# Kernel optimization log

Measured on AMD Instinct MI355X. Metric: run time of the kernel, lower is better.

Reference implementation:

```python
import jax, jax.numpy as jnp
import numpy as np

# static config (matches init_kwargs and spatial_shapes input)
SPATIAL = ((100, 100), (50, 50), (25, 25), (13, 13))  # (H, W) per level
D_MODEL, N_HEADS, N_LEVELS, N_POINTS, D_FFN = 256, 8, 4, 4, 1024
D_HEAD = D_MODEL // N_HEADS
LEN_IN = sum(h * w for h, w in SPATIAL)
LEVEL_START = np.cumsum([0] + [h * w for h, w in SPATIAL])[:-1]


def setup_inputs() -> dict:
    key = jax.random.key(0)
    ks = jax.random.split(key, 12)
    N = 2
    f = lambda k, shape, s=0.02: jax.random.normal(k, shape, jnp.float32) * s
    return {
        "src": jax.random.normal(ks[0], (N, LEN_IN, D_MODEL), jnp.float32),
        "pos": jax.random.normal(ks[1], (N, LEN_IN, D_MODEL), jnp.float32),
        "reference_points": jax.random.uniform(ks[2], (N, LEN_IN, N_LEVELS, 2), jnp.float32),
        "spatial_shapes": jnp.asarray(SPATIAL, jnp.int32),
        "level_start_index": jnp.asarray(LEVEL_START, jnp.int32),
        "W_value": f(ks[3], (D_MODEL, D_MODEL)),
        "b_value": jnp.zeros((D_MODEL,), jnp.float32),
        "W_off": f(ks[4], (D_MODEL, N_HEADS * N_LEVELS * N_POINTS * 2)),
        "b_off": f(ks[5], (N_HEADS * N_LEVELS * N_POINTS * 2,), 0.5),
        "W_attn": f(ks[6], (D_MODEL, N_HEADS * N_LEVELS * N_POINTS)),
        "b_attn": jnp.zeros((N_HEADS * N_LEVELS * N_POINTS,), jnp.float32),
        "W_out": f(ks[7], (D_MODEL, D_MODEL)),
        "b_out": jnp.zeros((D_MODEL,), jnp.float32),
        "W1": f(ks[8], (D_MODEL, D_FFN)),
        "b1": jnp.zeros((D_FFN,), jnp.float32),
        "W2": f(ks[9], (D_FFN, D_MODEL)),
        "b2": jnp.zeros((D_MODEL,), jnp.float32),
        "g1": jnp.ones((D_MODEL,), jnp.float32),
        "be1": jnp.zeros((D_MODEL,), jnp.float32),
        "g2": jnp.ones((D_MODEL,), jnp.float32),
        "be2": jnp.zeros((D_MODEL,), jnp.float32),
    }


def _ln(x, g, b, eps=1e-5):
    mu = x.mean(-1, keepdims=True)
    var = ((x - mu) ** 2).mean(-1, keepdims=True)
    return (x - mu) * jax.lax.rsqrt(var + eps) * g + b


def _bilinear(v, loc, H, W):
    # v: [N, heads, H*W, Dh]; loc: [N, Lq, heads, P, 2] normalized to [0,1]
    # replicates F.grid_sample(align_corners=False, padding_mode='zeros') with grid=2*loc-1
    N, Lq, Hh, P, _ = loc.shape
    x = loc[..., 0] * W - 0.5
    y = loc[..., 1] * H - 0.5
    x0 = jnp.floor(x)
    y0 = jnp.floor(y)
    wx1 = x - x0
    wy1 = y - y0
    x0i = x0.astype(jnp.int32)
    y0i = y0.astype(jnp.int32)
    out = jnp.zeros((N, Lq, Hh, P, v.shape[-1]), v.dtype)
    for dy, dx in ((0, 0), (0, 1), (1, 0), (1, 1)):
        xi = x0i + dx
        yi = y0i + dy
        w = (wx1 if dx else 1.0 - wx1) * (wy1 if dy else 1.0 - wy1)
        valid = (xi >= 0) & (xi < W) & (yi >= 0) & (yi < H)
        idx = jnp.clip(yi, 0, H - 1) * W + jnp.clip(xi, 0, W - 1)  # [N,Lq,Hh,P]
        idx = idx.transpose(0, 2, 1, 3).reshape(N, Hh, Lq * P)
        g = jax.vmap(jax.vmap(lambda vm, im: vm[im]))(v, idx)  # [N,Hh,Lq*P,Dh]
        g = g.reshape(N, Hh, Lq, P, -1).transpose(0, 2, 1, 3, 4)
        out = out + (w * valid)[..., None] * g
    return out


def reference(src, pos, reference_points, spatial_shapes, level_start_index,
              W_value, b_value, W_off, b_off, W_attn, b_attn, W_out, b_out,
              W1, b1, W2, b2, g1, be1, g2, be2):
    N, Lq, _ = src.shape
    value = (src @ W_value + b_value).reshape(N, Lq, N_HEADS, D_HEAD)
    q = src + pos  # with_pos_embed
    off = (q @ W_off + b_off).reshape(N, Lq, N_HEADS, N_LEVELS, N_POINTS, 2)
    attn = (q @ W_attn + b_attn).reshape(N, Lq, N_HEADS, N_LEVELS * N_POINTS)
    attn = jax.nn.softmax(attn, axis=-1).reshape(N, Lq, N_HEADS, N_LEVELS, N_POINTS)
    # offset_normalizer = (W, H) per level
    normalizer = jnp.asarray([[w, h] for h, w in SPATIAL], jnp.float32)
    loc = reference_points[:, :, None, :, None, :] + off / normalizer[None, None, None, :, None, :]
    out = jnp.zeros((N, Lq, N_HEADS, D_HEAD), jnp.float32)
    for l, (H, W) in enumerate(SPATIAL):
        s = int(LEVEL_START[l])
        v_l = value[:, s:s + H * W].transpose(0, 2, 1, 3)  # [N, heads, H*W, Dh]
        samp = _bilinear(v_l, loc[:, :, :, l], H, W)       # [N, Lq, heads, P, Dh]
        out = out + jnp.einsum('nqhp,nqhpc->nqhc', attn[:, :, :, l], samp)
    src2 = out.reshape(N, Lq, D_MODEL) @ W_out + b_out
    x = _ln(src + src2, g1, be1)
    ffn = jax.nn.relu(x @ W1 + b1) @ W2 + b2
    return _ln(x + ffn, g2, be2)
```

## Files before the change

kernel.cpp:

```cpp
#include <hip/hip_runtime.h>
#include <hip/hip_bf16.h>
#include <cstdint>

#define D_MODEL   256
#define N_HEADS   8
#define N_LEVELS  4
#define N_POINTS  4
#define D_FFN     1024
#define D_HEAD    32
#define LEN_IN    13294
#define NBATCH    2
#define M_TOK     (NBATCH * LEN_IN)
#define M_PAD     26624

__constant__ int c_lvl_h[4] = {100, 50, 25, 13};
__constant__ int c_lvl_w[4] = {100, 50, 25, 13};
__constant__ int c_lvl_s[4] = {0, 10000, 12500, 13125};

typedef __attribute__((ext_vector_type(8))) __bf16 bf16x8;
typedef __attribute__((ext_vector_type(4))) __bf16 bf16x4;
typedef __attribute__((ext_vector_type(4))) float  f32x4;
typedef __attribute__((ext_vector_type(4))) uint32_t u32x4;

__device__ __forceinline__ float bflo(uint32_t w) { return __uint_as_float(w << 16); }
__device__ __forceinline__ float bfhi(uint32_t w) { return __uint_as_float(w & 0xffff0000u); }

__device__ __forceinline__ void lds_direct16(const void* g, void* l) {
    __builtin_amdgcn_global_load_lds(
        (const __attribute__((address_space(1))) uint32_t*)(uintptr_t)g,
        (__attribute__((address_space(3))) uint32_t*)(uintptr_t)l,
        16, 0, 0);
}

__global__ __launch_bounds__(256) void prep(
    const float* __restrict__ s0, const float* __restrict__ s1, const float* __restrict__ s2,
    const float* __restrict__ s3, const float* __restrict__ s4, const float* __restrict__ s5,
    __bf16* __restrict__ d0, __bf16* __restrict__ d1, __bf16* __restrict__ d2,
    __bf16* __restrict__ d3, __bf16* __restrict__ d4, __bf16* __restrict__ d5,
    const float* __restrict__ b_off, const float* __restrict__ b_attn,
    float* __restrict__ bias_oa,
    const float4* __restrict__ src, const float4* __restrict__ pos,
    bf16x4* __restrict__ sb, bf16x4* __restrict__ qb, int n4)
{
    const int tid = threadIdx.x;
    const int b = blockIdx.x;
    if (b >= 737) {
        const int i = (b - 737) * 256 + tid;
        if (i >= n4) return;
        const float4 s = src[i];
        const float4 p = pos[i];
        bf16x4 sv = { (__bf16)s.x, (__bf16)s.y, (__bf16)s.z, (__bf16)s.w };
        bf16x4 qv = { (__bf16)(s.x + p.x), (__bf16)(s.y + p.y),
                      (__bf16)(s.z + p.z), (__bf16)(s.w + p.w) };
        sb[i] = sv;
        qb[i] = qv;
        return;
    }
    if (b == 736) {
        if (tid < 256) bias_oa[tid] = b_off[tid];
        if (tid < 128) bias_oa[256 + tid] = b_attn[tid];
        return;
    }
    const int tx = tid & 31;
    const int ty = tid >> 5;
    const int starts[7] = {0, 64, 128, 160, 224, 480, 736};
    const int Ks[6] = {256, 256, 256, 256, 256, 1024};
    const int Ns[6] = {256, 256, 128, 256, 1024, 256};
    const float* srcs[6] = {s0, s1, s2, s3, s4, s5};
    __bf16* dsts[6] = {d0, d1, d2, d3, d4, d5};
    int i = 0;
    while (b >= starts[i + 1]) ++i;
    const int t = b - starts[i];
    const int K = Ks[i], N = Ns[i];
    const float* W = srcs[i];
    __bf16* Wt = dsts[i];
    const int ntx = N >> 5;
    const int n0 = (t % ntx) * 32;
    const int k0 = (t / ntx) * 32;

    __shared__ float tl[32][33];
    #pragma unroll
    for (int j = 0; j < 4; ++j)
        tl[ty + j * 8][tx] = W[(size_t)(k0 + ty + j * 8) * N + n0 + tx];
    __syncthreads();
    #pragma unroll
    for (int j = 0; j < 4; ++j)
        Wt[(size_t)(n0 + ty + j * 8) * K + k0 + tx] = (__bf16)tl[tx][ty + j * 8];
}

template <bool RELU, int K>
__device__ __forceinline__ void gemm_core(
    const __bf16* __restrict__ A, const __bf16* __restrict__ Bt,
    const float* __restrict__ bias, __bf16* __restrict__ C,
    int M, int N, int bm, int bn)
{
    __shared__ __bf16 smem[17408];
    __bf16* As = smem;
    __bf16* Bs = smem + 8192;

    const int tid  = threadIdx.x;
    const int lane = tid & 63;
    const int wv   = tid >> 6;
    const int wm   = (wv >> 1) * 64;
    const int wn   = (wv & 1) * 64;
    const int srow = lane >> 2;
    const int skc  = (lane & 3) * 8;
    const int fm   = lane & 15;
    const int fko  = (lane >> 4) * 8;

    f32x4 acc[4][4] = {};

    for (int k0 = 0; k0 < K; k0 += 64) {
        #pragma unroll
        for (int p = 0; p < 2; ++p) {
            #pragma unroll
            for (int c = 0; c < 2; ++c) {
                const int r = wv * 32 + c * 16;
                lds_direct16(A  + (size_t)(bm + r + srow) * K + k0 + p * 32 + skc, As + p * 4096 + r * 32);
                lds_direct16(Bt + (size_t)(bn + r + srow) * K + k0 + p * 32 + skc, Bs + p * 4096 + r * 32);
            }
        }
        __syncthreads();

        #pragma unroll
        for (int p = 0; p < 2; ++p) {
            bf16x8 af[4], bfr[4];
            #pragma unroll
            for (int t = 0; t < 4; ++t) {
                af[t]  = *(const bf16x8*)(As + p * 4096 + (wm + t * 16 + fm) * 32 + fko);
                bfr[t] = *(const bf16x8*)(Bs + p * 4096 + (wn + t * 16 + fm) * 32 + fko);
            }
            #pragma unroll
            for (int mt = 0; mt < 4; ++mt)
                #pragma unroll
                for (int nt = 0; nt < 4; ++nt)
                    acc[mt][nt] = __builtin_amdgcn_mfma_f32_16x16x32_bf16(
                        af[mt], bfr[nt], acc[mt][nt], 0, 0, 0);
        }
        __syncthreads();
    }

    const int ecol = lane & 15;
    const int erow = (lane >> 4) * 4;
    #pragma unroll
    for (int nt = 0; nt < 4; ++nt) {
        const int cl = wn + nt * 16 + ecol;
        const float bv = bias[bn + cl];
        #pragma unroll
        for (int mt = 0; mt < 4; ++mt) {
            #pragma unroll
            for (int r = 0; r < 4; ++r) {
                const int rl = wm + mt * 16 + erow + r;
                float v = acc[mt][nt][r] + bv;
                if (RELU) v = fmaxf(v, 0.f);
                smem[rl * 136 + cl] = (__bf16)v;
            }
        }
    }
    __syncthreads();
    #pragma unroll
    for (int rr = 0; rr < 8; ++rr) {
        const int idx = rr * 256 + tid;
        const int row = idx >> 4;
        const int ch  = idx & 15;
        if (bm + row < M)
            *(bf16x8*)(C + (size_t)(bm + row) * N + bn + ch * 8) =
                *(const bf16x8*)(smem + row * 136 + ch * 8);
    }
}

__global__ __launch_bounds__(256) void gemm_front(
    const __bf16* __restrict__ A0, const __bf16* __restrict__ B0,
    const float* __restrict__ bi0, __bf16* __restrict__ C0,
    const __bf16* __restrict__ A1, const __bf16* __restrict__ B1,
    const float* __restrict__ bi1, __bf16* __restrict__ C1, int M)
{
    const int bx = blockIdx.x;
    if (bx < 2)
        gemm_core<false, 256>(A0, B0, bi0, C0, M, 256, blockIdx.y * 128, bx * 128);
    else
        gemm_core<false, 256>(A1, B1, bi1, C1, M, 384, blockIdx.y * 128, (bx - 2) * 128);
}

__global__ __launch_bounds__(256) void gemm_ffn1(
    const __bf16* __restrict__ A, const __bf16* __restrict__ Bt,
    const float* __restrict__ bias, __bf16* __restrict__ C, int M)
{
    gemm_core<true, 256>(A, Bt, bias, C, M, 1024, blockIdx.y * 128, blockIdx.x * 128);
}

template <typename OutT, int K>
__global__ __launch_bounds__(256) void gemm_ln32(
    const __bf16* __restrict__ A, const __bf16* __restrict__ Bt,
    const float* __restrict__ bias, const __bf16* __restrict__ res,
    const float* __restrict__ gamma, const float* __restrict__ beta,
    OutT* __restrict__ Cout, int M)
{
    __shared__ __bf16 smem[18432];
    __bf16* As = smem;
    __bf16* Bs = smem + 2048;
    __shared__ float lnsum[32][4];
    __shared__ float lnsq[32][4];
    __shared__ float lnstat[32][2];

    const int tid  = threadIdx.x;
    const int lane = tid & 63;
    const int wv   = tid >> 6;
    const int bm   = blockIdx.x * 32;
    const int wn   = wv * 64;
    const int srow = lane >> 2;
    const int skc  = (lane & 3) * 8;
    const int fm   = lane & 15;
    const int fko  = (lane >> 4) * 8;

    f32x4 acc[2][4] = {};

    for (int k0 = 0; k0 < K; k0 += 64) {
        {
            const int p  = wv >> 1;
            const int rh = (wv & 1) * 16;
            lds_direct16(A + (size_t)(bm + rh + srow) * K + k0 + p * 32 + skc,
                         As + p * 1024 + rh * 32);
        }
        #pragma unroll
        for (int p = 0; p < 2; ++p) {
            #pragma unroll
            for (int c = 0; c < 4; ++c) {
                const int r = wv * 64 + c * 16;
                lds_direct16(Bt + (size_t)(r + srow) * K + k0 + p * 32 + skc,
                             Bs + p * 8192 + r * 32);
            }
        }
        __syncthreads();

        #pragma unroll
        for (int p = 0; p < 2; ++p) {
            bf16x8 af[2], bfr[4];
            #pragma unroll
            for (int mt = 0; mt < 2; ++mt)
                af[mt] = *(const bf16x8*)(As + p * 1024 + (mt * 16 + fm) * 32 + fko);
            #pragma unroll
            for (int nt = 0; nt < 4; ++nt)
                bfr[nt] = *(const bf16x8*)(Bs + p * 8192 + (wn + nt * 16 + fm) * 32 + fko);
            #pragma unroll
            for (int mt = 0; mt < 2; ++mt)
                #pragma unroll
                for (int nt = 0; nt < 4; ++nt)
                    acc[mt][nt] = __builtin_amdgcn_mfma_f32_16x16x32_bf16(
                        af[mt], bfr[nt], acc[mt][nt], 0, 0, 0);
        }
        __syncthreads();
    }

    const int ecol = lane & 15;
    const int erow = (lane >> 4) * 4;

    float g4[4], b4[4];
    #pragma unroll
    for (int nt = 0; nt < 4; ++nt) {
        const int col = wn + nt * 16 + ecol;
        g4[nt] = gamma[col];
        b4[nt] = beta[col];
        const float bv = bias[col];
        #pragma unroll
        for (int mt = 0; mt < 2; ++mt) {
            #pragma unroll
            for (int r = 0; r < 4; ++r) {
                const int row = bm + mt * 16 + erow + r;
                acc[mt][nt][r] += bv + (float)res[(size_t)row * 256 + col];
            }
        }
    }

    #pragma unroll
    for (int mt = 0; mt < 2; ++mt) {
        #pragma unroll
        for (int r = 0; r < 4; ++r) {
            float s  = acc[mt][0][r] + acc[mt][1][r] + acc[mt][2][r] + acc[mt][3][r];
            float s2 = acc[mt][0][r] * acc[mt][0][r] + acc[mt][1][r] * acc[mt][1][r]
                     + acc[mt][2][r] * acc[mt][2][r] + acc[mt][3][r] * acc[mt][3][r];
            #pragma unroll
            for (int o = 1; o < 16; o <<= 1) {
                s  += __shfl_xor(s, o);
                s2 += __shfl_xor(s2, o);
            }
            if (ecol == 0) {
                const int rl = mt * 16 + erow + r;
                lnsum[rl][wv] = s;
                lnsq[rl][wv]  = s2;
            }
        }
    }
    __syncthreads();
    if (tid < 32) {
        const float s  = lnsum[tid][0] + lnsum[tid][1] + lnsum[tid][2] + lnsum[tid][3];
        const float s2 = lnsq[tid][0] + lnsq[tid][1] + lnsq[tid][2] + lnsq[tid][3];
        const float mu = s * (1.f / 256.f);
        const float var = s2 * (1.f / 256.f) - mu * mu;
        lnstat[tid][0] = mu;
        lnstat[tid][1] = rsqrtf(var + 1e-5f);
    }
    __syncthreads();

    if constexpr (sizeof(OutT) == 2) {
        __bf16* ct = smem;
        #pragma unroll
        for (int mt = 0; mt < 2; ++mt) {
            #pragma unroll
            for (int r = 0; r < 4; ++r) {
                const int rl = mt * 16 + erow + r;
                const float mu = lnstat[rl][0];
                const float rs = lnstat[rl][1];
                #pragma unroll
                for (int nt = 0; nt < 4; ++nt) {
                    const int col = wn + nt * 16 + ecol;
                    ct[rl * 264 + col] = (__bf16)((acc[mt][nt][r] - mu) * rs * g4[nt] + b4[nt]);
                }
            }
        }
        __syncthreads();
        #pragma unroll
        for (int rr = 0; rr < 4; ++rr) {
            const int idx = rr * 256 + tid;
            const int row = idx >> 5;
            const int ch  = idx & 31;
            if (bm + row < M)
                *(bf16x8*)((__bf16*)Cout + (size_t)(bm + row) * 256 + ch * 8) =
                    *(const bf16x8*)(ct + row * 264 + ch * 8);
        }
    } else {
        float* ct = (float*)smem;
        #pragma unroll
        for (int mt = 0; mt < 2; ++mt) {
            #pragma unroll
            for (int r = 0; r < 4; ++r) {
                const int rl = mt * 16 + erow + r;
                const float mu = lnstat[rl][0];
                const float rs = lnstat[rl][1];
                #pragma unroll
                for (int nt = 0; nt < 4; ++nt) {
                    const int col = wn + nt * 16 + ecol;
                    ct[rl * 260 + col] = (acc[mt][nt][r] - mu) * rs * g4[nt] + b4[nt];
                }
            }
        }
        __syncthreads();
        #pragma unroll
        for (int rr = 0; rr < 8; ++rr) {
            const int idx = rr * 256 + tid;
            const int row = idx >> 6;
            const int ch  = idx & 63;
            if (bm + row < M) {
                float4 v = *(const float4*)(ct + row * 260 + ch * 4);
                *(float4*)((float*)Cout + (size_t)(bm + row) * 256 + ch * 4) = v;
            }
        }
    }
}

__global__ __launch_bounds__(256) void msda_sample(
    const __bf16* __restrict__ value,
    const __bf16* __restrict__ oa,
    const float* __restrict__ refp,
    __bf16* __restrict__ out)
{
    __shared__ uint32_t sc[64 * 132];
    __shared__ float sw[64][16];

    const int tid = threadIdx.x;
    const int blk = blockIdx.x;

    if (tid < 64) {
        const int t = tid >> 3;
        const int h = tid & 7;
        int row = blk * 8 + t; if (row >= M_TOK) row = M_TOK - 1;
        const __bf16* ap = oa + (size_t)row * 384 + 256 + h * 16;
        const bf16x8 v0 = *(const bf16x8*)ap;
        const bf16x8 v1 = *(const bf16x8*)(ap + 8);
        float e[16];
        #pragma unroll
        for (int i = 0; i < 8; ++i) { e[i] = (float)v0[i]; e[8 + i] = (float)v1[i]; }
        float mx = -1e30f;
        #pragma unroll
        for (int i = 0; i < 16; ++i) mx = fmaxf(mx, e[i]);
        float s = 0.f;
        #pragma unroll
        for (int i = 0; i < 16; ++i) { e[i] = __expf(e[i] - mx); s += e[i]; }
        const float inv = 1.f / s;
        #pragma unroll
        for (int i = 0; i < 16; ++i) sw[tid][i] = e[i] * inv;
    }
    __syncthreads();

    #pragma unroll
    for (int it = 0; it < 4; ++it) {
        const int idx = it * 256 + tid;
        const int t  = idx >> 7;
        const int h  = (idx >> 4) & 7;
        const int lp = idx & 15;
        const int l  = lp >> 2;
        int row = blk * 8 + t; if (row >= M_TOK) row = M_TOK - 1;
        const int Ww = c_lvl_w[l];
        const int Hh = c_lvl_h[l];
        const uint32_t opk = *(const uint32_t*)(oa + (size_t)row * 384 + h * 32 + lp * 2);
        const float ox = bflo(opk), oy = bfhi(opk);
        const float rx = refp[((size_t)row * 4 + l) * 2 + 0];
        const float ry = refp[((size_t)row * 4 + l) * 2 + 1];
        const float x = (rx + ox / (float)Ww) * (float)Ww - 0.5f;
        const float y = (ry + oy / (float)Hh) * (float)Hh - 0.5f;
        const float xf = floorf(x), yf = floorf(y);
        const float fx = x - xf,    fy = y - yf;
        const int x0 = (int)xf, y0 = (int)yf;
        const int n  = row / LEN_IN;
        const int base = n * LEN_IN + c_lvl_s[l];
        const float a = sw[t * 8 + h][lp];
        uint32_t cidx[4];
        float    cwt[4];
        #pragma unroll
        for (int c = 0; c < 4; ++c) {
            const int dx = c & 1, dy = c >> 1;
            const int xi = x0 + dx, yi = y0 + dy;
            const bool valid = (xi >= 0) & (xi < Ww) & (yi >= 0) & (yi < Hh);
            cidx[c] = valid ? (uint32_t)(base + yi * Ww + xi) * 512u : 0u;
            cwt[c]  = valid ? (dx ? fx : 1.f - fx) * (dy ? fy : 1.f - fy) * a : 0.f;
        }
        uint32_t* p = sc + (t * 8 + h) * 132 + lp * 8;
        u32x4 pk0 = { cidx[0], __float_as_uint(cwt[0]), cidx[1], __float_as_uint(cwt[1]) };
        u32x4 pk1 = { cidx[2], __float_as_uint(cwt[2]), cidx[3], __float_as_uint(cwt[3]) };
        *(u32x4*)p = pk0;
        *(u32x4*)(p + 4) = pk1;
    }
    __syncthreads();

    const int t  = tid >> 5;
    const int h  = (tid >> 2) & 7;
    const int c4 = tid & 3;
    const uint32_t colb = (uint32_t)(h * 64 + c4 * 16);
    const uint32_t* mb = sc + (t * 8 + h) * 132;
    const char* __restrict__ vb = (const char*)value;
    float acc[8] = {};
    #pragma unroll
    for (int q = 0; q < 16; ++q) {
        const u32x4 A = *(const u32x4*)(mb + q * 8);
        const u32x4 B = *(const u32x4*)(mb + q * 8 + 4);
        const uint32_t ix[4] = { A.x, A.z, B.x, B.z };
        const uint32_t wb[4] = { A.y, A.w, B.y, B.w };
        #pragma unroll
        for (int c = 0; c < 4; ++c) {
            const float w = __uint_as_float(wb[c]);
            const u32x4 v = *(const u32x4*)(vb + (size_t)(ix[c] + colb));
            #pragma unroll
            for (int d = 0; d < 4; ++d) {
                acc[2 * d]     += w * bflo(v[d]);
                acc[2 * d + 1] += w * bfhi(v[d]);
            }
        }
    }
    const int orow = blk * 8 + t;
    bf16x8 o;
    #pragma unroll
    for (int j = 0; j < 8; ++j) o[j] = (__bf16)acc[j];
    *(bf16x8*)(out + (size_t)orow * 256 + colb / 2) = o;
}

extern "C" void kernel_launch(void* const* d_in, const int* in_sizes, int n_in,
                              void* d_out, int out_size, void* d_ws, size_t ws_size,
                              hipStream_t stream)
{
    const float* src     = (const float*)d_in[0];
    const float* pos     = (const float*)d_in[1];
    const float* refp    = (const float*)d_in[2];
    const float* W_value = (const float*)d_in[5];
    const float* b_value = (const float*)d_in[6];
    const float* W_off   = (const float*)d_in[7];
    const float* b_off   = (const float*)d_in[8];
    const float* W_attn  = (const float*)d_in[9];
    const float* b_attn  = (const float*)d_in[10];
    const float* W_out   = (const float*)d_in[11];
    const float* b_out   = (const float*)d_in[12];
    const float* W1      = (const float*)d_in[13];
    const float* b1      = (const float*)d_in[14];
    const float* W2      = (const float*)d_in[15];
    const float* b2      = (const float*)d_in[16];
    const float* g1      = (const float*)d_in[17];
    const float* be1     = (const float*)d_in[18];
    const float* g2      = (const float*)d_in[19];
    const float* be2     = (const float*)d_in[20];
    float* outp = (float*)d_out;

    const int M = M_TOK;
    char* ws = (char*)d_ws;
    const size_t R2 = (size_t)M_PAD * 512;

    __bf16* src_b = (__bf16*)(ws);
    __bf16* q_b   = (__bf16*)(ws + R2);
    __bf16* val_b = (__bf16*)(ws + 2 * R2);
    __bf16* oa    = (__bf16*)(ws + 3 * R2);
    __bf16* samp  = (__bf16*)(ws + 9 * R2 / 2);
    __bf16* x_b   = (__bf16*)(ws + 11 * R2 / 2);
    __bf16* hbuf  = (__bf16*)(ws);
    __bf16* wbase = (__bf16*)(ws + 13 * R2 / 2);
    __bf16* Wt_value = wbase;
    __bf16* Wt_oa    = wbase + 65536;
    __bf16* Wt_out   = wbase + 163840;
    __bf16* Wt1      = wbase + 229376;
    __bf16* Wt2      = wbase + 491520;
    float*  bias_oa  = (float*)(wbase + 753664);

    const dim3 blk(256);
    const int n4 = M * 256 / 4;
    const int gm = M_PAD / 128;

    prep<<<dim3(737 + (n4 + 255) / 256), blk, 0, stream>>>(
        W_value, W_off, W_attn, W_out, W1, W2,
        Wt_value, Wt_oa, Wt_oa + 65536, Wt_out, Wt1, Wt2,
        b_off, b_attn, bias_oa,
        (const float4*)src, (const float4*)pos, (bf16x4*)src_b, (bf16x4*)q_b, n4);

    gemm_front<<<dim3(5, gm), blk, 0, stream>>>(
        src_b, Wt_value, b_value, val_b,
        q_b,   Wt_oa,    bias_oa, oa, M);

    msda_sample<<<dim3((M + 7) / 8), blk, 0, stream>>>(val_b, oa, refp, samp);

    gemm_ln32<__bf16, 256><<<dim3(M_PAD / 32), blk, 0, stream>>>(
        samp, Wt_out, b_out, src_b, g1, be1, x_b, M);

    gemm_ffn1<<<dim3(8, gm), blk, 0, stream>>>(x_b, Wt1, b1, hbuf, M);

    gemm_ln32<float, 1024><<<dim3(M_PAD / 32), blk, 0, stream>>>(
        hbuf, Wt2, b2, x_b, g2, be2, outp, M);
}
```

Baseline: 297.3 us.

## Store value projection head-major and sample bilinear row pairs per load

The value GEMM now writes its output in a head-major layout ([head][token][32]), so each head's value rows are contiguous 64-byte records. The sampling kernel clamps x to Ww-2 and fetches each bilinear row pair (two adjacent pixels) with one 128-byte span split across 8 lanes. The lanes holding the left and right pixel are then combined with a shuffle. Blocks process 4 queries instead of 8, doubling the grid. The aim is fewer, more coalesced gathers and less metadata, at the cost of cross-lane reduction and more blocks. The kernel also depends on M being divisible by 4 and on val_b being sized to M_PAD*256.

```diff
diff --git a/kernel.cpp b/kernel.cpp
--- a/kernel.cpp
+++ b/kernel.cpp
@@ -88,7 +88,7 @@
         Wt[(size_t)(n0 + ty + j * 8) * K + k0 + tx] = (__bf16)tl[tx][ty + j * 8];
 }
 
-template <bool RELU, int K>
+template <bool RELU, int K, bool HEADMAJOR>
 __device__ __forceinline__ void gemm_core(
     const __bf16* __restrict__ A, const __bf16* __restrict__ Bt,
     const float* __restrict__ bias, __bf16* __restrict__ C,
@@ -163,9 +163,16 @@
         const int idx = rr * 256 + tid;
         const int row = idx >> 4;
         const int ch  = idx & 15;
-        if (bm + row < M)
-            *(bf16x8*)(C + (size_t)(bm + row) * N + bn + ch * 8) =
-                *(const bf16x8*)(smem + row * 136 + ch * 8);
+        if (bm + row < M) {
+            if (HEADMAJOR) {
+                const int col = bn + ch * 8;
+                *(bf16x8*)(C + ((size_t)(col >> 5) * M_PAD + (bm + row)) * 32 + (col & 31)) =
+                    *(const bf16x8*)(smem + row * 136 + ch * 8);
+            } else {
+                *(bf16x8*)(C + (size_t)(bm + row) * N + bn + ch * 8) =
+                    *(const bf16x8*)(smem + row * 136 + ch * 8);
+            }
+        }
     }
 }
 
@@ -177,16 +184,16 @@
 {
     const int bx = blockIdx.x;
     if (bx < 2)
-        gemm_core<false, 256>(A0, B0, bi0, C0, M, 256, blockIdx.y * 128, bx * 128);
+        gemm_core<false, 256, true>(A0, B0, bi0, C0, M, 256, blockIdx.y * 128, bx * 128);
     else
-        gemm_core<false, 256>(A1, B1, bi1, C1, M, 384, blockIdx.y * 128, (bx - 2) * 128);
+        gemm_core<false, 256, false>(A1, B1, bi1, C1, M, 384, blockIdx.y * 128, (bx - 2) * 128);
 }
 
 __global__ __launch_bounds__(256) void gemm_ffn1(
     const __bf16* __restrict__ A, const __bf16* __restrict__ Bt,
     const float* __restrict__ bias, __bf16* __restrict__ C, int M)
 {
-    gemm_core<true, 256>(A, Bt, bias, C, M, 1024, blockIdx.y * 128, blockIdx.x * 128);
+    gemm_core<true, 256, false>(A, Bt, bias, C, M, 1024, blockIdx.y * 128, blockIdx.x * 128);
 }
 
 template <typename OutT, int K>
@@ -364,16 +371,16 @@
     const float* __restrict__ refp,
     __bf16* __restrict__ out)
 {
-    __shared__ uint32_t sc[64 * 132];
-    __shared__ float sw[64][16];
+    __shared__ uint32_t sc[32 * 132];
+    __shared__ float sw[32][16];
 
     const int tid = threadIdx.x;
     const int blk = blockIdx.x;
 
-    if (tid < 64) {
+    if (tid < 32) {
         const int t = tid >> 3;
         const int h = tid & 7;
-        int row = blk * 8 + t; if (row >= M_TOK) row = M_TOK - 1;
+        const int row = blk * 4 + t;
         const __bf16* ap = oa + (size_t)row * 384 + 256 + h * 16;
         const bf16x8 v0 = *(const bf16x8*)ap;
         const bf16x8 v1 = *(const bf16x8*)(ap + 8);
@@ -393,13 +400,13 @@
     __syncthreads();
 
     #pragma unroll
-    for (int it = 0; it < 4; ++it) {
+    for (int it = 0; it < 2; ++it) {
         const int idx = it * 256 + tid;
         const int t  = idx >> 7;
         const int h  = (idx >> 4) & 7;
         const int lp = idx & 15;
         const int l  = lp >> 2;
-        int row = blk * 8 + t; if (row >= M_TOK) row = M_TOK - 1;
+        const int row = blk * 4 + t;
         const int Ww = c_lvl_w[l];
         const int Hh = c_lvl_h[l];
         const uint32_t opk = *(const uint32_t*)(oa + (size_t)row * 384 + h * 32 + lp * 2);
@@ -411,56 +418,56 @@
         const float xf = floorf(x), yf = floorf(y);
         const float fx = x - xf,    fy = y - yf;
         const int x0 = (int)xf, y0 = (int)yf;
-        const int n  = row / LEN_IN;
-        const int base = n * LEN_IN + c_lvl_s[l];
+        const int n  = (row >= LEN_IN) ? 1 : 0;
+        const int lvlbase = n * LEN_IN + c_lvl_s[l];
         const float a = sw[t * 8 + h][lp];
-        uint32_t cidx[4];
-        float    cwt[4];
-        #pragma unroll
-        for (int c = 0; c < 4; ++c) {
-            const int dx = c & 1, dy = c >> 1;
-            const int xi = x0 + dx, yi = y0 + dy;
-            const bool valid = (xi >= 0) & (xi < Ww) & (yi >= 0) & (yi < Hh);
-            cidx[c] = valid ? (uint32_t)(base + yi * Ww + xi) * 512u : 0u;
-            cwt[c]  = valid ? (dx ? fx : 1.f - fx) * (dy ? fy : 1.f - fy) * a : 0.f;
-        }
+        const int xs = min(max(x0, 0), Ww - 2);
+        const int d  = x0 - xs;
+        const float wxl = 1.f - fx, wxr = fx;
+        const float pw0 = (d == 0) ? wxl : ((d == -1) ? wxr : 0.f);
+        const float pw1 = (d == 0) ? wxr : ((d == 1) ? wxl : 0.f);
         uint32_t* p = sc + (t * 8 + h) * 132 + lp * 8;
-        u32x4 pk0 = { cidx[0], __float_as_uint(cwt[0]), cidx[1], __float_as_uint(cwt[1]) };
-        u32x4 pk1 = { cidx[2], __float_as_uint(cwt[2]), cidx[3], __float_as_uint(cwt[3]) };
-        *(u32x4*)p = pk0;
-        *(u32x4*)(p + 4) = pk1;
+        #pragma unroll
+        for (int dy = 0; dy < 2; ++dy) {
+            const int yi = y0 + dy;
+            const int yc = min(max(yi, 0), Hh - 1);
+            const bool yv = (yi >= 0) & (yi < Hh);
+            const float wy = (dy ? fy : 1.f - fy) * (yv ? a : 0.f);
+            const uint32_t boff = (uint32_t)(lvlbase + yc * Ww + xs) * 64u;
+            u32x4 pk = { boff, __float_as_uint(pw0 * wy), __float_as_uint(pw1 * wy), 0u };
+            *(u32x4*)(p + dy * 4) = pk;
+        }
     }
     __syncthreads();
 
-    const int t  = tid >> 5;
-    const int h  = (tid >> 2) & 7;
-    const int c4 = tid & 3;
-    const uint32_t colb = (uint32_t)(h * 64 + c4 * 16);
+    const int t  = tid >> 6;
+    const int h  = (tid >> 3) & 7;
+    const int c8 = tid & 7;
     const uint32_t* mb = sc + (t * 8 + h) * 132;
-    const char* __restrict__ vb = (const char*)value;
+    const char* __restrict__ vpb = (const char*)(value + (size_t)h * (M_PAD * 32));
+    const uint32_t lsub = (uint32_t)c8 * 16u;
+    const bool hi = (c8 >= 4);
     float acc[8] = {};
-    #pragma unroll
-    for (int q = 0; q < 16; ++q) {
-        const u32x4 A = *(const u32x4*)(mb + q * 8);
-        const u32x4 B = *(const u32x4*)(mb + q * 8 + 4);
-        const uint32_t ix[4] = { A.x, A.z, B.x, B.z };
-        const uint32_t wb[4] = { A.y, A.w, B.y, B.w };
-        #pragma unroll
-        for (int c = 0; c < 4; ++c) {
-            const float w = __uint_as_float(wb[c]);
-            const u32x4 v = *(const u32x4*)(vb + (size_t)(ix[c] + colb));
-            #pragma unroll
-            for (int d = 0; d < 4; ++d) {
-                acc[2 * d]     += w * bflo(v[d]);
-                acc[2 * d + 1] += w * bfhi(v[d]);
-            }
-        }
-    }
-    const int orow = blk * 8 + t;
-    bf16x8 o;
-    #pragma unroll
-    for (int j = 0; j < 8; ++j) o[j] = (__bf16)acc[j];
-    *(bf16x8*)(out + (size_t)orow * 256 + colb / 2) = o;
+    #pragma unroll 8
+    for (int qd = 0; qd < 32; ++qd) {
+        const u32x4 md = *(const u32x4*)(mb + qd * 4);
+        const float w = __uint_as_float(hi ? md.z : md.y);
+        const u32x4 v = *(const u32x4*)(vpb + (size_t)(md.x + lsub));
+        #pragma unroll
+        for (int d2 = 0; d2 < 4; ++d2) {
+            acc[2 * d2]     += w * bflo(v[d2]);
+            acc[2 * d2 + 1] += w * bfhi(v[d2]);
+        }
+    }
+    #pragma unroll
+    for (int j = 0; j < 8; ++j) acc[j] += __shfl_xor(acc[j], 4);
+    if (c8 < 4) {
+        bf16x8 o;
+        #pragma unroll
+        for (int j = 0; j < 8; ++j) o[j] = (__bf16)acc[j];
+        const int orow = blk * 4 + t;
+        *(bf16x8*)(out + (size_t)orow * 256 + h * 32 + c8 * 8) = o;
+    }
 }
 
 extern "C" void kernel_launch(void* const* d_in, const int* in_sizes, int n_in,
@@ -521,7 +528,7 @@
         src_b, Wt_value, b_value, val_b,
         q_b,   Wt_oa,    bias_oa, oa, M);
 
-    msda_sample<<<dim3((M + 7) / 8), blk, 0, stream>>>(val_b, oa, refp, samp);
+    msda_sample<<<dim3(M / 4), blk, 0, stream>>>(val_b, oa, refp, samp);
 
     gemm_ln32<__bf16, 256><<<dim3(M_PAD / 32), blk, 0, stream>>>(
         samp, Wt_out, b_out, src_b, g1, be1, x_b, M);
```

Result: no change. 299.2 us (+0.6%).
